# Optimization experiments

Measured on AMD Instinct MI355X. Metric: run time of the kernel, lower is better.

Reference implementation:

```python
import jax, jax.numpy as jnp
import numpy as np

B_, S_, D_ = 2, 2048, 2048
H_, KV_ = 16, 4
HD_ = D_ // H_          # 128
R_ = H_ // KV_          # GQA repeat factor
MLP_ = 4 * D_
ROPE_BASE = 10000.0
TRAIN_SEQ = 1024


def _rms(x):
    eps = jnp.finfo(x.dtype).eps
    return x * jax.lax.rsqrt(jnp.mean(jnp.square(x), axis=-1, keepdims=True) + eps)


def _rope_tables(S, d):
    # Rotary.forward: NTK base rescale when seq_len > train_seq_len
    if S > TRAIN_SEQ:
        scale = S / TRAIN_SEQ
        base = ROPE_BASE * scale ** (d / (d - 2))
    else:
        base = ROPE_BASE
    inv_freq = 1.0 / base ** (np.arange(0, d, 2, dtype=np.float32) / d)
    t = np.arange(S, dtype=np.float32)
    fr = np.outer(t, inv_freq)              # [S, d//2]
    return jnp.asarray(np.cos(fr)), jnp.asarray(np.sin(fr))


def _apply_rope(x, cos, sin):
    # x: [B,S,h,d]; full-dim rotation (rope_dims == head_dim)
    h = x.shape[-1] // 2
    x1, x2 = x[..., :h], x[..., h:]
    c = cos[None, :, None, :]
    s = sin[None, :, None, :]
    return jnp.concatenate([x1 * c + x2 * s, -x1 * s + x2 * c], axis=-1)


def setup_inputs() -> dict:
    key = jax.random.key(0)
    ks = jax.random.split(key, 12)
    wstd = 0.02
    inp = {
        'x':  jax.random.normal(ks[0], (B_, S_, D_), jnp.float32),
        'x0': jax.random.normal(ks[1], (B_, S_, D_), jnp.float32),
        'q_w':   jax.random.normal(ks[2], (D_, D_), jnp.float32) * wstd,
        'k_w':   jax.random.normal(ks[3], (KV_ * HD_, D_), jnp.float32) * wstd,
        'v_w':   jax.random.normal(ks[4], (KV_ * HD_, D_), jnp.float32) * wstd,
        'out_w': jax.random.normal(ks[5], (D_, D_), jnp.float32) * wstd,
        'up_w':   jax.random.normal(ks[6], (MLP_, D_), jnp.float32) * wstd,
        'down_w': jax.random.normal(ks[7], (D_, MLP_), jnp.float32) * wstd,
        'v_embed': jax.random.normal(ks[8], (B_, S_, KV_ * HD_), jnp.float32) * 0.05,
        'v0': jax.random.normal(ks[9], (B_, S_, KV_, HD_), jnp.float32),
        'q_gain': jnp.ones((H_,), jnp.float32),                  # qk_gain_init = 1.0
        'attn_gate_w': jax.random.normal(ks[10], (H_, D_), jnp.float32) * 0.01,
        'attn_gate_b': jnp.full((H_,), 4.0, jnp.float32),        # init constant 4.0
        'vr_lambda': jnp.array([0.5, 0.5], jnp.float32),
        'attn_scale': jnp.ones((D_,), jnp.float32),
        'mlp_scale': jnp.ones((D_,), jnp.float32),
        'resid_mix': jnp.stack([jnp.ones((D_,)), jnp.zeros((D_,))]).astype(jnp.float32)
                     + jax.random.normal(ks[11], (2, D_), jnp.float32) * 0.01,
    }
    return inp


def reference(x, x0, q_w, k_w, v_w, out_w, up_w, down_w, v_embed, v0,
              q_gain, attn_gate_w, attn_gate_b, vr_lambda,
              attn_scale, mlp_scale, resid_mix):
    B, S, D = x.shape
    # residual mix of current and initial embedding streams
    xm = resid_mix[0][None, None, :] * x + resid_mix[1][None, None, :] * x0
    h = _rms(xm)  # attn_norm, ln_scale_factor == 1

    # ---- attention ----
    q = (h @ q_w.T).reshape(B, S, H_, HD_)
    k = (h @ k_w.T).reshape(B, S, KV_, HD_)
    v = (h @ v_w.T) + v_embed
    v = v.reshape(B, S, KV_, HD_)
    v_resid = v  # returned for value-residual of later layers
    v = vr_lambda[0] * v0 + vr_lambda[1] * v

    q = _rms(q)
    k = _rms(k)
    cos, sin = _rope_tables(S, HD_)
    q = _apply_rope(q, cos, sin)
    k = _apply_rope(k, cos, sin)
    q = q * q_gain[None, None, :, None]

    # GQA causal SDPA; head h maps to kv group h // R_ (repeat_interleave order)
    qg = q.reshape(B, S, KV_, R_, HD_)
    scores = jnp.einsum('bqkrd,bskd->bkrqs', qg, k) / jnp.sqrt(jnp.asarray(HD_, x.dtype))
    causal = jnp.tril(jnp.ones((S, S), dtype=bool))
    scores = jnp.where(causal[None, None, None, :, :], scores, -jnp.inf)
    attn = jax.nn.softmax(scores, axis=-1)
    y = jnp.einsum('bkrqs,bskd->bqkrd', attn, v)  # [B,S,KV,R,HD]

    # _xsa_efficient: remove component of y along normalized v direction (per kv group)
    vh = v / jnp.clip(jnp.linalg.norm(v, axis=-1, keepdims=True), 1e-12)
    vh = vh[:, :, :, None, :]
    y = y - jnp.sum(y * vh, axis=-1, keepdims=True) * vh

    # per-head sigmoid gate computed from the normed block input
    gate = jax.nn.sigmoid(h @ attn_gate_w.T + attn_gate_b)  # [B,S,H]
    y = y * gate.reshape(B, S, KV_, R_, 1)

    attn_out = y.reshape(B, S, D) @ out_w.T
    c = xm + attn_scale[None, None, :] * attn_out

    # ---- MLP: leaky_relu(0.5) then square, per MLP.forward ----
    m = _rms(c)
    u = m @ up_w.T
    u = jnp.where(u >= 0, u, 0.5 * u)
    mlp_out = jnp.square(u) @ down_w.T
    c = c + mlp_scale[None, None, :] * mlp_out
    return c, v_resid
```

## Files before the change

kernel.cpp:

```cpp
#include <hip/hip_runtime.h>
#include <hip/hip_bf16.h>
#include <cfloat>

#define B_ 2
#define S_ 2048
#define D_ 2048
#define H_ 16
#define KV_ 4
#define HD_ 128
#define R_ 4
#define MLP_ 8192
#define N_ (B_*S_)

typedef unsigned short ushort_t;
typedef __bf16 bf16x8 __attribute__((ext_vector_type(8)));
typedef float f32x4 __attribute__((ext_vector_type(4)));

__device__ __forceinline__ float b2f(ushort_t u) {
    unsigned x = ((unsigned)u) << 16;
    return __builtin_bit_cast(float, x);
}
__device__ __forceinline__ ushort_t f2b(float f) {
    unsigned u = __builtin_bit_cast(unsigned, f);
    unsigned r = (u + 0x7fffu + ((u >> 16) & 1u)) >> 16;
    return (ushort_t)r;
}

__device__ __forceinline__ void gload_lds16(const void* g, void* l) {
    __builtin_amdgcn_global_load_lds(
        (__attribute__((address_space(1))) void*)(g),
        (__attribute__((address_space(3))) void*)(l), 16, 0, 0);
}

__global__ __launch_bounds__(256) void f2bf_kernel(const float* __restrict__ in,
                                                   ushort_t* __restrict__ out, int n4)
{
    int i = blockIdx.x * 256 + threadIdx.x;
    if (i < n4) {
        float4 v = ((const float4*)in)[i];
        ushort4 o;
        o.x = f2b(v.x); o.y = f2b(v.y); o.z = f2b(v.z); o.w = f2b(v.w);
        ((ushort4*)out)[i] = o;
    }
}

template<bool MIX>
__global__ __launch_bounds__(256) void rms_kernel(
    const float* __restrict__ x, const float* __restrict__ x0,
    const float* __restrict__ rm, float* __restrict__ xm_out,
    ushort_t* __restrict__ h_out)
{
    int n = blockIdx.x;
    int tid = threadIdx.x;
    const float4* xr = (const float4*)(x + (size_t)n * D_);
    float4 v[2];
    float ss = 0.f;
#pragma unroll
    for (int i = 0; i < 2; i++) {
        int c = tid + i * 256;
        float4 a = xr[c];
        if (MIX) {
            const float4* x0r = (const float4*)(x0 + (size_t)n * D_);
            const float4* rma = (const float4*)rm;
            const float4* rmb = (const float4*)(rm + D_);
            float4 b = x0r[c];
            float4 ra = rma[c], rb = rmb[c];
            a.x = ra.x*a.x + rb.x*b.x;
            a.y = ra.y*a.y + rb.y*b.y;
            a.z = ra.z*a.z + rb.z*b.z;
            a.w = ra.w*a.w + rb.w*b.w;
            ((float4*)(xm_out + (size_t)n * D_))[c] = a;
        }
        v[i] = a;
        ss += a.x*a.x + a.y*a.y + a.z*a.z + a.w*a.w;
    }
#pragma unroll
    for (int off = 32; off; off >>= 1) ss += __shfl_xor(ss, off);
    __shared__ float red[4];
    if ((tid & 63) == 0) red[tid >> 6] = ss;
    __syncthreads();
    float tot = red[0] + red[1] + red[2] + red[3];
    float r = rsqrtf(tot * (1.f / (float)D_) + FLT_EPSILON);
    ushort4* ho = (ushort4*)(h_out + (size_t)n * D_);
#pragma unroll
    for (int i = 0; i < 2; i++) {
        int c = tid + i * 256;
        float4 a = v[i];
        ushort4 o;
        o.x = f2b(a.x * r); o.y = f2b(a.y * r); o.z = f2b(a.z * r); o.w = f2b(a.w * r);
        ho[c] = o;
    }
}

template<int EPI, typename OutT>
__global__ __launch_bounds__(256) void gemm_bf16(
    const ushort_t* __restrict__ A, const ushort_t* __restrict__ W,
    OutT* __restrict__ C, int M, int Kd,
    const float* __restrict__ src, const float* __restrict__ svec)
{
    __shared__ ushort_t As[128 * 32];
    __shared__ ushort_t Bs[128 * 32];
    const int tid = threadIdx.x;
    const int wid = tid >> 6, lane = tid & 63;
    const int bn = blockIdx.y * 128;
    const int bm = blockIdx.x * 128;
    const int wn = (wid >> 1) * 64;
    const int wm = (wid & 1) * 64;

    f32x4 acc[4][4] = {};

    const int lr = lane & 15;
    const int lk = (lane >> 4) * 16;
    const char* Ab = (const char*)As;
    const char* Bb = (const char*)Bs;
    const int ub0 = wid * 128;

#pragma unroll
    for (int p = 0; p < 2; p++) {
        int ub = ub0 + p * 64;
        int u = ub + lane;
        gload_lds16(A + (size_t)(bn + (u >> 2)) * Kd + (u & 3) * 8, (char*)As + ub * 16);
        gload_lds16(W + (size_t)(bm + (u >> 2)) * Kd + (u & 3) * 8, (char*)Bs + ub * 16);
    }
    __syncthreads();

    for (int k0 = 0;;) {
        bf16x8 af[4], bfr[4];
#pragma unroll
        for (int i = 0; i < 4; i++)
            af[i] = *(const bf16x8*)(Ab + (wn + i * 16 + lr) * 64 + lk);
#pragma unroll
        for (int j = 0; j < 4; j++)
            bfr[j] = *(const bf16x8*)(Bb + (wm + j * 16 + lr) * 64 + lk);
#pragma unroll
        for (int i = 0; i < 4; i++)
#pragma unroll
            for (int j = 0; j < 4; j++)
                acc[i][j] = __builtin_amdgcn_mfma_f32_16x16x32_bf16(af[i], bfr[j], acc[i][j], 0, 0, 0);

        k0 += 32;
        if (k0 >= Kd) break;
        __syncthreads();
#pragma unroll
        for (int p = 0; p < 2; p++) {
            int ub = ub0 + p * 64;
            int u = ub + lane;
            gload_lds16(A + (size_t)(bn + (u >> 2)) * Kd + k0 + (u & 3) * 8, (char*)As + ub * 16);
            gload_lds16(W + (size_t)(bm + (u >> 2)) * Kd + k0 + (u & 3) * 8, (char*)Bs + ub * 16);
        }
        __syncthreads();
    }

    const int cr = (lane >> 4) * 4;
    const int ccol = lane & 15;
#pragma unroll
    for (int i = 0; i < 4; i++) {
#pragma unroll
        for (int r = 0; r < 4; r++) {
            size_t rowoff = (size_t)(bn + wn + i * 16 + cr + r) * M;
#pragma unroll
            for (int j = 0; j < 4; j++) {
                int m = bm + wm + j * 16 + ccol;
                size_t off = rowoff + m;
                float v = acc[i][j][r];
                if (EPI == 1) v += src[off];
                else if (EPI == 2) v = src[off] + svec[m] * v;
                else if (EPI == 3) { float t = v >= 0.f ? v : 0.5f * v; v = t * t; }
                if constexpr (sizeof(OutT) == 2) C[off] = (OutT)f2b(v);
                else                             C[off] = v;
            }
        }
    }
}

__global__ __launch_bounds__(256) void vmix_kernel(
    const float* __restrict__ vres, const float* __restrict__ v0,
    const float* __restrict__ lam, ushort_t* __restrict__ vm)
{
    int i = blockIdx.x * 256 + threadIdx.x;
    float l0 = lam[0], l1 = lam[1];
    float4 a = ((const float4*)vres)[i];
    float4 b = ((const float4*)v0)[i];
    ushort4 o;
    o.x = f2b(l0*b.x + l1*a.x);
    o.y = f2b(l0*b.y + l1*a.y);
    o.z = f2b(l0*b.z + l1*a.z);
    o.w = f2b(l0*b.w + l1*a.w);
    ((ushort4*)vm)[i] = o;
}

__global__ __launch_bounds__(256) void vtrans_kernel(const ushort_t* __restrict__ vm,
                                                     ushort_t* __restrict__ vt)
{
    int s = blockIdx.x * 64 + (threadIdx.x & 63);
    int c0 = blockIdx.y * 32 + (threadIdx.x >> 6) * 8;
    int b = blockIdx.z;
    uint4 raw = *(const uint4*)(vm + (size_t)(b * S_ + s) * (KV_*HD_) + c0);
    ushort_t tmp[8];
    *(uint4*)tmp = raw;
#pragma unroll
    for (int i = 0; i < 8; i++)
        vt[((size_t)b * (KV_*HD_) + c0 + i) * S_ + s] = tmp[i];
}

__global__ __launch_bounds__(128) void ropeqk_kernel(
    ushort_t* __restrict__ q, ushort_t* __restrict__ k,
    const float* __restrict__ q_gain)
{
    int n = blockIdx.x;
    int head = blockIdx.y;
    int tid = threadIdx.x;
    bool isq = head < H_;
    ushort_t* vec = isq ? (q + (size_t)n * D_ + head * HD_)
                        : (k + (size_t)n * (KV_*HD_) + (head - H_) * HD_);
    float v = b2f(vec[tid]);
    float ss = v * v;
#pragma unroll
    for (int off = 32; off; off >>= 1) ss += __shfl_xor(ss, off);
    __shared__ float red[2];
    __shared__ float sh[HD_];
    if ((tid & 63) == 0) red[tid >> 6] = ss;
    __syncthreads();
    float tot = red[0] + red[1];
    float r = rsqrtf(tot * (1.f / (float)HD_) + FLT_EPSILON);
    float xn = v * r;
    sh[tid] = xn;
    __syncthreads();
    int s = n & (S_ - 1);
    int i = (tid < 64) ? tid : tid - 64;
    const float L2B = 14.303585395422465f;
    float invf = exp2f(-(float)i * (L2B / 64.f));
    float fr = (float)s * invf;
    float c = cosf(fr), sn = sinf(fr);
    float out;
    if (tid < 64) out =  xn * c + sh[tid + 64] * sn;
    else          out = -sh[tid - 64] * sn + xn * c;
    if (isq) out *= q_gain[head];
    vec[tid] = f2b(out);
}

__global__ __launch_bounds__(256) void attn_mfma_kernel(
    const ushort_t* __restrict__ Qg, const ushort_t* __restrict__ Kg,
    const ushort_t* __restrict__ Vtg, ushort_t* __restrict__ Y)
{
    const int b = blockIdx.z, h = blockIdx.y;
    const int kv = h >> 2;
    const int qb = blockIdx.x * 64;
    const int tid = threadIdx.x;
    const int wid = tid >> 6, lane = tid & 63;
    const int l15 = lane & 15, quad = lane >> 4;

    __shared__ ushort_t Ks[4 * 64 * 32];
    __shared__ ushort_t Vs[2 * 128 * 32];
    __shared__ ushort_t Ps[4][2 * 16 * 32];

    bf16x8 qf[4];
    {
        const ushort_t* qrow = Qg + (size_t)(b * S_ + qb + wid * 16 + l15) * D_ + h * HD_ + quad * 8;
#pragma unroll
        for (int kc = 0; kc < 4; kc++)
            qf[kc] = __builtin_bit_cast(bf16x8, *(const uint4*)(qrow + kc * 32));
    }

    f32x4 O[8];
    float m_r[4], l_r[4];
#pragma unroll
    for (int dt = 0; dt < 8; dt++)
#pragma unroll
        for (int r = 0; r < 4; r++) O[dt][r] = 0.f;
#pragma unroll
    for (int r = 0; r < 4; r++) { m_r[r] = -1e30f; l_r[r] = 0.f; }

    const size_t kgbase = (size_t)b * S_ * (KV_*HD_) + kv * HD_;
    const size_t vgbase = (size_t)(b * KV_ + kv) * HD_ * S_;
    const float CS = 0.12751743f;

    const int ntiles = blockIdx.x + 1;
    for (int t = 0; t < ntiles; t++) {
        const int k0 = t * 64;
        if (t) __syncthreads();
#pragma unroll
        for (int p = 0; p < 4; p++) {
            int ub = wid * 256 + p * 64 + lane;
            int kc = ub >> 8, j = (ub >> 2) & 63, q = ub & 3;
            gload_lds16(Kg + kgbase + (size_t)(k0 + j) * (KV_*HD_) + kc * 32 + q * 8,
                        (char*)Ks + ub * 16);
            int jc = ub >> 9, d = (ub >> 2) & 127;
            gload_lds16(Vtg + vgbase + (size_t)d * S_ + k0 + jc * 32 + q * 8,
                        (char*)Vs + ub * 16);
        }
        __syncthreads();

        f32x4 sc[4];
#pragma unroll
        for (int jt = 0; jt < 4; jt++)
#pragma unroll
            for (int r = 0; r < 4; r++) sc[jt][r] = 0.f;
#pragma unroll
        for (int kc = 0; kc < 4; kc++) {
#pragma unroll
            for (int jt = 0; jt < 4; jt++) {
                bf16x8 kf = *(const bf16x8*)(Ks + kc * 2048 + (jt * 16 + l15) * 32 + quad * 8);
                sc[jt] = __builtin_amdgcn_mfma_f32_16x16x32_bf16(qf[kc], kf, sc[jt], 0, 0, 0);
            }
        }

        float pv[4][4];
        const bool diag = (t == ntiles - 1);
#pragma unroll
        for (int jt = 0; jt < 4; jt++)
#pragma unroll
            for (int r = 0; r < 4; r++) {
                float s = sc[jt][r] * CS;
                if (diag && (jt * 16 + l15 > wid * 16 + quad * 4 + r)) s = -1e30f;
                pv[jt][r] = s;
            }
        float al[4];
#pragma unroll
        for (int r = 0; r < 4; r++) {
            float m0 = fmaxf(fmaxf(pv[0][r], pv[1][r]), fmaxf(pv[2][r], pv[3][r]));
#pragma unroll
            for (int o = 1; o < 16; o <<= 1) m0 = fmaxf(m0, __shfl_xor(m0, o));
            float mn = fmaxf(m_r[r], m0);
            al[r] = exp2f(m_r[r] - mn);
            m_r[r] = mn;
            float srow = 0.f;
#pragma unroll
            for (int jt = 0; jt < 4; jt++) { pv[jt][r] = exp2f(pv[jt][r] - mn); srow += pv[jt][r]; }
#pragma unroll
            for (int o = 1; o < 16; o <<= 1) srow += __shfl_xor(srow, o);
            l_r[r] = l_r[r] * al[r] + srow;
        }
#pragma unroll
        for (int dt = 0; dt < 8; dt++)
#pragma unroll
            for (int r = 0; r < 4; r++) O[dt][r] *= al[r];

        ushort_t* pw = Ps[wid];
#pragma unroll
        for (int jt = 0; jt < 4; jt++)
#pragma unroll
            for (int r = 0; r < 4; r++)
                pw[(jt >> 1) * 512 + (quad * 4 + r) * 32 + (jt & 1) * 16 + l15] = f2b(pv[jt][r]);

#pragma unroll
        for (int jc = 0; jc < 2; jc++) {
            bf16x8 pf = *(const bf16x8*)(pw + jc * 512 + l15 * 32 + quad * 8);
#pragma unroll
            for (int dt = 0; dt < 8; dt++) {
                bf16x8 vf = *(const bf16x8*)(Vs + jc * 4096 + (dt * 16 + l15) * 32 + quad * 8);
                O[dt] = __builtin_amdgcn_mfma_f32_16x16x32_bf16(pf, vf, O[dt], 0, 0, 0);
            }
        }
    }

#pragma unroll
    for (int r = 0; r < 4; r++) {
        float inv = 1.f / l_r[r];
        size_t row = (size_t)(b * S_ + qb + wid * 16 + quad * 4 + r) * D_ + h * HD_;
#pragma unroll
        for (int dt = 0; dt < 8; dt++)
            Y[row + dt * 16 + l15] = f2b(O[dt][r] * inv);
    }
}

__global__ __launch_bounds__(256) void postproc_kernel(
    const ushort_t* __restrict__ h, const ushort_t* __restrict__ vmix,
    const float* __restrict__ gw, const float* __restrict__ gb,
    ushort_t* __restrict__ y)
{
    int n = blockIdx.x;
    int tid = threadIdx.x;
    int wave = tid >> 6, lane = tid & 63;
    const ushort_t* hrow = h + (size_t)n * D_;
    float acc[4] = {0.f, 0.f, 0.f, 0.f};
    for (int d = lane; d < D_; d += 64) {
        float hv = b2f(hrow[d]);
#pragma unroll
        for (int r = 0; r < 4; r++)
            acc[r] += hv * gw[(size_t)(wave*4 + r) * D_ + d];
    }
#pragma unroll
    for (int off = 32; off; off >>= 1)
#pragma unroll
        for (int r = 0; r < 4; r++) acc[r] += __shfl_xor(acc[r], off);
    float gate[4];
#pragma unroll
    for (int r = 0; r < 4; r++)
        gate[r] = 1.f / (1.f + __expf(-(acc[r] + gb[wave*4 + r])));
    const ushort_t* vrow = vmix + (size_t)n * (KV_*HD_) + wave * HD_;
    float v0 = b2f(vrow[lane]), v1 = b2f(vrow[lane + 64]);
    float ss = v0*v0 + v1*v1;
#pragma unroll
    for (int off = 32; off; off >>= 1) ss += __shfl_xor(ss, off);
    float nrm = fmaxf(sqrtf(ss), 1e-12f);
    float vh0 = v0 / nrm, vh1 = v1 / nrm;
    ushort_t* yrow = y + (size_t)n * D_ + wave * (R_ * HD_);
#pragma unroll
    for (int r = 0; r < 4; r++) {
        float y0 = b2f(yrow[r*HD_ + lane]), y1 = b2f(yrow[r*HD_ + lane + 64]);
        float dot = y0*vh0 + y1*vh1;
#pragma unroll
        for (int off = 32; off; off >>= 1) dot += __shfl_xor(dot, off);
        yrow[r*HD_ + lane]      = f2b((y0 - dot*vh0) * gate[r]);
        yrow[r*HD_ + lane + 64] = f2b((y1 - dot*vh1) * gate[r]);
    }
}

extern "C" void kernel_launch(void* const* d_in, const int* in_sizes, int n_in,
                              void* d_out, int out_size, void* d_ws, size_t ws_size,
                              hipStream_t stream) {
    const float* x          = (const float*)d_in[0];
    const float* x0         = (const float*)d_in[1];
    const float* q_w        = (const float*)d_in[2];
    const float* k_w        = (const float*)d_in[3];
    const float* v_w        = (const float*)d_in[4];
    const float* out_w      = (const float*)d_in[5];
    const float* up_w       = (const float*)d_in[6];
    const float* down_w     = (const float*)d_in[7];
    const float* v_embed    = (const float*)d_in[8];
    const float* v0         = (const float*)d_in[9];
    const float* q_gain     = (const float*)d_in[10];
    const float* gate_w     = (const float*)d_in[11];
    const float* gate_b     = (const float*)d_in[12];
    const float* vr_lambda  = (const float*)d_in[13];
    const float* attn_scale = (const float*)d_in[14];
    const float* mlp_scale  = (const float*)d_in[15];
    const float* resid_mix  = (const float*)d_in[16];

    float* out_c  = (float*)d_out;
    float* out_vr = out_c + (size_t)N_ * D_;

    char* w = (char*)d_ws;
    ushort_t* hb  = (ushort_t*)(w + 0);
    float*    xm  = (float*)   (w + 16777216);
    ushort_t* qb  = (ushort_t*)(w + 50331648);
    ushort_t* kb  = (ushort_t*)(w + 67108864);
    ushort_t* vmb = (ushort_t*)(w + 71303168);
    ushort_t* yb  = (ushort_t*)(w + 75497472);
    ushort_t* wq  = (ushort_t*)(w + 92274688);
    ushort_t* wk  = (ushort_t*)(w + 100663296);
    ushort_t* wv  = (ushort_t*)(w + 102760448);
    ushort_t* wo  = (ushort_t*)(w + 104857600);
    ushort_t* vtb = (ushort_t*)(w + 113246208);
    ushort_t* act = (ushort_t*)(w + 16777216);
    ushort_t* wu  = (ushort_t*)(w + 83886080);
    ushort_t* wd  = (ushort_t*)(w + 117440512);
    ushort_t* m2  = (ushort_t*)(w + 0);

    f2bf_kernel<<<4096, 256, 0, stream>>>(q_w,    wq, 2048*2048/4);
    f2bf_kernel<<<1024, 256, 0, stream>>>(k_w,    wk,  512*2048/4);
    f2bf_kernel<<<1024, 256, 0, stream>>>(v_w,    wv,  512*2048/4);
    f2bf_kernel<<<4096, 256, 0, stream>>>(out_w,  wo, 2048*2048/4);
    f2bf_kernel<<<16384,256, 0, stream>>>(down_w, wd, 2048*8192/4);

    rms_kernel<true><<<N_, 256, 0, stream>>>(x, x0, resid_mix, xm, hb);
    gemm_bf16<0, ushort_t><<<dim3(16, 32), 256, 0, stream>>>(hb, wq, qb, D_, D_, nullptr, nullptr);
    gemm_bf16<0, ushort_t><<<dim3(4, 32), 256, 0, stream>>>(hb, wk, kb, KV_*HD_, D_, nullptr, nullptr);
    gemm_bf16<1, float><<<dim3(4, 32), 256, 0, stream>>>(hb, wv, out_vr, KV_*HD_, D_, v_embed, nullptr);
    vmix_kernel<<<(N_*KV_*HD_/4)/256, 256, 0, stream>>>(out_vr, v0, vr_lambda, vmb);
    vtrans_kernel<<<dim3(S_/64, (KV_*HD_)/32, B_), 256, 0, stream>>>(vmb, vtb);
    ropeqk_kernel<<<dim3(N_, H_ + KV_), 128, 0, stream>>>(qb, kb, q_gain);
    attn_mfma_kernel<<<dim3(S_/64, H_, B_), 256, 0, stream>>>(qb, kb, vtb, yb);
    postproc_kernel<<<N_, 256, 0, stream>>>(hb, vmb, gate_w, gate_b, yb);
    gemm_bf16<2, float><<<dim3(16, 32), 256, 0, stream>>>(yb, wo, out_c, D_, D_, xm, attn_scale);
    f2bf_kernel<<<16384, 256, 0, stream>>>(up_w, wu, 8192*2048/4);
    rms_kernel<false><<<N_, 256, 0, stream>>>(out_c, nullptr, nullptr, nullptr, m2);
    gemm_bf16<3, ushort_t><<<dim3(64, 32), 256, 0, stream>>>(m2, wu, act, MLP_, D_, nullptr, nullptr);
    gemm_bf16<2, float><<<dim3(16, 32), 256, 0, stream>>>(act, wd, out_c, D_, MLP_, out_c, mlp_scale);
}
```

Measured before the change: 1.079 ms.

## Fuse QKV GEMMs with RoPE, v-mix and transpose epilogue; swizzle tiles

The separate Q, K and V projection GEMMs become one launch over the contiguous bf16 weight buffers. A per-tile epilogue applies the per-head RMS norm, RoPE and q_gain to Q/K, and for V adds v_embed, does the lambda mix and writes both the row-major and transposed copies. This removes the vmix, vtrans and ropeqk kernels and their extra global round-trips. GEMM blocks are also remapped with an XCD-aware swizzle, and attention blocks are launched longest-first to shorten the causal tail. The costs are a heavier epilogue with extra LDS, scattered transposed stores, and per-element sin/cos in the GEMM.

```diff
diff --git a/kernel.cpp b/kernel.cpp
--- a/kernel.cpp
+++ b/kernel.cpp
@@ -30,6 +30,15 @@
     __builtin_amdgcn_global_load_lds(
         (__attribute__((address_space(1))) void*)(g),
         (__attribute__((address_space(3))) void*)(l), 16, 0, 0);
+}
+
+__device__ __forceinline__ void xcd_swizzle(int& bx, int& by) {
+    int gx = gridDim.x, gy = gridDim.y;
+    int flat = blockIdx.y * gx + blockIdx.x;
+    int G = gx * gy;
+    int n = (flat & 7) * (G >> 3) + (flat >> 3);
+    bx = n / gy;
+    by = n % gy;
 }
 
 __global__ __launch_bounds__(256) void f2bf_kernel(const float* __restrict__ in,
@@ -102,8 +111,10 @@
     __shared__ ushort_t Bs[128 * 32];
     const int tid = threadIdx.x;
     const int wid = tid >> 6, lane = tid & 63;
-    const int bn = blockIdx.y * 128;
-    const int bm = blockIdx.x * 128;
+    int bxs, bys;
+    xcd_swizzle(bxs, bys);
+    const int bn = bys * 128;
+    const int bm = bxs * 128;
     const int wn = (wid >> 1) * 64;
     const int wm = (wid & 1) * 64;
 
@@ -173,70 +184,160 @@
     }
 }
 
-__global__ __launch_bounds__(256) void vmix_kernel(
-    const float* __restrict__ vres, const float* __restrict__ v0,
-    const float* __restrict__ lam, ushort_t* __restrict__ vm)
+__global__ __launch_bounds__(256) void gemm_qkv(
+    const ushort_t* __restrict__ A, const ushort_t* __restrict__ W,
+    ushort_t* __restrict__ qb, ushort_t* __restrict__ kb,
+    float* __restrict__ out_vr, ushort_t* __restrict__ vmb, ushort_t* __restrict__ vtb,
+    const float* __restrict__ v_embed, const float* __restrict__ v0,
+    const float* __restrict__ q_gain, const float* __restrict__ vr_lambda)
 {
-    int i = blockIdx.x * 256 + threadIdx.x;
-    float l0 = lam[0], l1 = lam[1];
-    float4 a = ((const float4*)vres)[i];
-    float4 b = ((const float4*)v0)[i];
-    ushort4 o;
-    o.x = f2b(l0*b.x + l1*a.x);
-    o.y = f2b(l0*b.y + l1*a.y);
-    o.z = f2b(l0*b.z + l1*a.z);
-    o.w = f2b(l0*b.w + l1*a.w);
-    ((ushort4*)vm)[i] = o;
-}
-
-__global__ __launch_bounds__(256) void vtrans_kernel(const ushort_t* __restrict__ vm,
-                                                     ushort_t* __restrict__ vt)
-{
-    int s = blockIdx.x * 64 + (threadIdx.x & 63);
-    int c0 = blockIdx.y * 32 + (threadIdx.x >> 6) * 8;
-    int b = blockIdx.z;
-    uint4 raw = *(const uint4*)(vm + (size_t)(b * S_ + s) * (KV_*HD_) + c0);
-    ushort_t tmp[8];
-    *(uint4*)tmp = raw;
-#pragma unroll
-    for (int i = 0; i < 8; i++)
-        vt[((size_t)b * (KV_*HD_) + c0 + i) * S_ + s] = tmp[i];
-}
-
-__global__ __launch_bounds__(128) void ropeqk_kernel(
-    ushort_t* __restrict__ q, ushort_t* __restrict__ k,
-    const float* __restrict__ q_gain)
-{
-    int n = blockIdx.x;
-    int head = blockIdx.y;
-    int tid = threadIdx.x;
-    bool isq = head < H_;
-    ushort_t* vec = isq ? (q + (size_t)n * D_ + head * HD_)
-                        : (k + (size_t)n * (KV_*HD_) + (head - H_) * HD_);
-    float v = b2f(vec[tid]);
-    float ss = v * v;
-#pragma unroll
-    for (int off = 32; off; off >>= 1) ss += __shfl_xor(ss, off);
-    __shared__ float red[2];
-    __shared__ float sh[HD_];
-    if ((tid & 63) == 0) red[tid >> 6] = ss;
+    __shared__ ushort_t As[128 * 32];
+    __shared__ ushort_t Bs[128 * 32];
+    __shared__ float ssb[2][128];
+    __shared__ ushort_t xb[128][132];
+    const int tid = threadIdx.x;
+    const int wid = tid >> 6, lane = tid & 63;
+    int bxs, bys;
+    xcd_swizzle(bxs, bys);
+    const int bn = bys * 128;
+    const int bm = bxs * 128;
+    const int wn = (wid >> 1) * 64;
+    const int wm = (wid & 1) * 64;
+    const int l15 = lane & 15, quad = lane >> 4;
+    const int Kd = D_;
+
+    f32x4 acc[4][4] = {};
+    const int lr = lane & 15;
+    const int lk = (lane >> 4) * 16;
+    const char* Ab = (const char*)As;
+    const char* Bb = (const char*)Bs;
+    const int ub0 = wid * 128;
+
+#pragma unroll
+    for (int p = 0; p < 2; p++) {
+        int ub = ub0 + p * 64;
+        int u = ub + lane;
+        gload_lds16(A + (size_t)(bn + (u >> 2)) * Kd + (u & 3) * 8, (char*)As + ub * 16);
+        gload_lds16(W + (size_t)(bm + (u >> 2)) * Kd + (u & 3) * 8, (char*)Bs + ub * 16);
+    }
     __syncthreads();
-    float tot = red[0] + red[1];
-    float r = rsqrtf(tot * (1.f / (float)HD_) + FLT_EPSILON);
-    float xn = v * r;
-    sh[tid] = xn;
+
+    for (int k0 = 0;;) {
+        bf16x8 af[4], bfr[4];
+#pragma unroll
+        for (int i = 0; i < 4; i++)
+            af[i] = *(const bf16x8*)(Ab + (wn + i * 16 + lr) * 64 + lk);
+#pragma unroll
+        for (int j = 0; j < 4; j++)
+            bfr[j] = *(const bf16x8*)(Bb + (wm + j * 16 + lr) * 64 + lk);
+#pragma unroll
+        for (int i = 0; i < 4; i++)
+#pragma unroll
+            for (int j = 0; j < 4; j++)
+                acc[i][j] = __builtin_amdgcn_mfma_f32_16x16x32_bf16(af[i], bfr[j], acc[i][j], 0, 0, 0);
+        k0 += 32;
+        if (k0 >= Kd) break;
+        __syncthreads();
+#pragma unroll
+        for (int p = 0; p < 2; p++) {
+            int ub = ub0 + p * 64;
+            int u = ub + lane;
+            gload_lds16(A + (size_t)(bn + (u >> 2)) * Kd + k0 + (u & 3) * 8, (char*)As + ub * 16);
+            gload_lds16(W + (size_t)(bm + (u >> 2)) * Kd + k0 + (u & 3) * 8, (char*)Bs + ub * 16);
+        }
+        __syncthreads();
+    }
+
+    if (bm >= 2560) {
+        const int kv = (bm - 2560) >> 7;
+        const float l0 = vr_lambda[0], l1 = vr_lambda[1];
+#pragma unroll
+        for (int i = 0; i < 4; i++) {
+#pragma unroll
+            for (int r = 0; r < 4; r++) {
+                int row = wn + i * 16 + quad * 4 + r;
+                int n = bn + row;
+                int bidx = n >> 11, s = n & (S_ - 1);
+#pragma unroll
+                for (int j = 0; j < 4; j++) {
+                    int c512 = kv * HD_ + wm + j * 16 + l15;
+                    size_t off = (size_t)n * (KV_*HD_) + c512;
+                    float vr = acc[i][j][r] + v_embed[off];
+                    out_vr[off] = vr;
+                    float vm = l0 * v0[off] + l1 * vr;
+                    ushort_t vmh = f2b(vm);
+                    vmb[off] = vmh;
+                    vtb[((size_t)(bidx * (KV_*HD_) + c512)) * S_ + s] = vmh;
+                }
+            }
+        }
+        return;
+    }
+
+    const bool isq = (bm < 2048);
+    const int head = bm >> 7;
+    const float gain = isq ? q_gain[head] : 1.f;
+
+    f32x4 rms4[4];
+#pragma unroll
+    for (int i = 0; i < 4; i++) {
+        f32x4 sv = {0.f, 0.f, 0.f, 0.f};
+#pragma unroll
+        for (int j = 0; j < 4; j++)
+#pragma unroll
+            for (int r = 0; r < 4; r++) sv[r] += acc[i][j][r] * acc[i][j][r];
+#pragma unroll
+        for (int r = 0; r < 4; r++) {
+            float ss = sv[r];
+#pragma unroll
+            for (int o = 1; o < 16; o <<= 1) ss += __shfl_xor(ss, o);
+            if (l15 == 0) ssb[wid & 1][wn + i * 16 + quad * 4 + r] = ss;
+            sv[r] = ss;
+        }
+        rms4[i] = sv;
+    }
     __syncthreads();
-    int s = n & (S_ - 1);
-    int i = (tid < 64) ? tid : tid - 64;
+#pragma unroll
+    for (int i = 0; i < 4; i++) {
+#pragma unroll
+        for (int r = 0; r < 4; r++) {
+            int row = wn + i * 16 + quad * 4 + r;
+            float tot = ssb[0][row] + ssb[1][row];
+            rms4[i][r] = rsqrtf(tot * (1.f / (float)HD_) + FLT_EPSILON);
+        }
+#pragma unroll
+        for (int j = 0; j < 4; j++)
+#pragma unroll
+            for (int r = 0; r < 4; r++) {
+                int row = wn + i * 16 + quad * 4 + r;
+                xb[row][wm + j * 16 + l15] = f2b(acc[i][j][r] * rms4[i][r]);
+            }
+    }
+    __syncthreads();
     const float L2B = 14.303585395422465f;
-    float invf = exp2f(-(float)i * (L2B / 64.f));
-    float fr = (float)s * invf;
-    float c = cosf(fr), sn = sinf(fr);
-    float out;
-    if (tid < 64) out =  xn * c + sh[tid + 64] * sn;
-    else          out = -sh[tid - 64] * sn + xn * c;
-    if (isq) out *= q_gain[head];
-    vec[tid] = f2b(out);
+    ushort_t* dst = isq ? qb : kb;
+    const int dstride = isq ? D_ : (KV_*HD_);
+    const int dbase = isq ? bm : (bm - 2048);
+#pragma unroll
+    for (int j = 0; j < 4; j++) {
+        int dcol = wm + j * 16 + l15;
+        float invf = exp2f(-(float)(dcol & 63) * (L2B / 64.f));
+#pragma unroll
+        for (int i = 0; i < 4; i++) {
+#pragma unroll
+            for (int r = 0; r < 4; r++) {
+                int row = wn + i * 16 + quad * 4 + r;
+                int n = bn + row;
+                int s = n & (S_ - 1);
+                float fr = (float)s * invf;
+                float c = cosf(fr), sn = sinf(fr);
+                float xs = acc[i][j][r] * rms4[i][r];
+                float xp = b2f(xb[row][dcol ^ 64]);
+                float outv = (wm == 0) ? (xs * c + xp * sn) : (xs * c - xp * sn);
+                dst[(size_t)n * dstride + dbase + dcol] = f2b(outv * gain);
+            }
+        }
+    }
 }
 
 __global__ __launch_bounds__(256) void attn_mfma_kernel(
@@ -245,7 +346,8 @@
 {
     const int b = blockIdx.z, h = blockIdx.y;
     const int kv = h >> 2;
-    const int qb = blockIdx.x * 64;
+    const int bx = gridDim.x - 1 - blockIdx.x;
+    const int qrow0 = bx * 64;
     const int tid = threadIdx.x;
     const int wid = tid >> 6, lane = tid & 63;
     const int l15 = lane & 15, quad = lane >> 4;
@@ -256,7 +358,7 @@
 
     bf16x8 qf[4];
     {
-        const ushort_t* qrow = Qg + (size_t)(b * S_ + qb + wid * 16 + l15) * D_ + h * HD_ + quad * 8;
+        const ushort_t* qrow = Qg + (size_t)(b * S_ + qrow0 + wid * 16 + l15) * D_ + h * HD_ + quad * 8;
 #pragma unroll
         for (int kc = 0; kc < 4; kc++)
             qf[kc] = __builtin_bit_cast(bf16x8, *(const uint4*)(qrow + kc * 32));
@@ -275,7 +377,7 @@
     const size_t vgbase = (size_t)(b * KV_ + kv) * HD_ * S_;
     const float CS = 0.12751743f;
 
-    const int ntiles = blockIdx.x + 1;
+    const int ntiles = bx + 1;
     for (int t = 0; t < ntiles; t++) {
         const int k0 = t * 64;
         if (t) __syncthreads();
@@ -357,7 +459,7 @@
 #pragma unroll
     for (int r = 0; r < 4; r++) {
         float inv = 1.f / l_r[r];
-        size_t row = (size_t)(b * S_ + qb + wid * 16 + quad * 4 + r) * D_ + h * HD_;
+        size_t row = (size_t)(b * S_ + qrow0 + wid * 16 + quad * 4 + r) * D_ + h * HD_;
 #pragma unroll
         for (int dt = 0; dt < 8; dt++)
             Y[row + dt * 16 + l15] = f2b(O[dt][r] * inv);
@@ -455,12 +557,8 @@
     f2bf_kernel<<<16384,256, 0, stream>>>(down_w, wd, 2048*8192/4);
 
     rms_kernel<true><<<N_, 256, 0, stream>>>(x, x0, resid_mix, xm, hb);
-    gemm_bf16<0, ushort_t><<<dim3(16, 32), 256, 0, stream>>>(hb, wq, qb, D_, D_, nullptr, nullptr);
-    gemm_bf16<0, ushort_t><<<dim3(4, 32), 256, 0, stream>>>(hb, wk, kb, KV_*HD_, D_, nullptr, nullptr);
-    gemm_bf16<1, float><<<dim3(4, 32), 256, 0, stream>>>(hb, wv, out_vr, KV_*HD_, D_, v_embed, nullptr);
-    vmix_kernel<<<(N_*KV_*HD_/4)/256, 256, 0, stream>>>(out_vr, v0, vr_lambda, vmb);
-    vtrans_kernel<<<dim3(S_/64, (KV_*HD_)/32, B_), 256, 0, stream>>>(vmb, vtb);
-    ropeqk_kernel<<<dim3(N_, H_ + KV_), 128, 0, stream>>>(qb, kb, q_gain);
+    gemm_qkv<<<dim3(24, 32), 256, 0, stream>>>(hb, wq, qb, kb, out_vr, vmb, vtb,
+                                               v_embed, v0, q_gain, vr_lambda);
     attn_mfma_kernel<<<dim3(S_/64, H_, B_), 256, 0, stream>>>(qb, kb, vtb, yb);
     postproc_kernel<<<N_, 256, 0, stream>>>(hb, vmb, gate_w, gate_b, yb);
     gemm_bf16<2, float><<<dim3(16, 32), 256, 0, stream>>>(yb, wo, out_c, D_, D_, xm, attn_scale);
```

After: 1.919 ms. 1.78x slower.
